# Kernel tuning notes

Hardware: AMD Instinct MI355X
Metric: run time of the kernel (lower is better)

The kernel has to match this reference:

```python
import jax, jax.numpy as jnp
import numpy as np

EPS = 1e-8  # torch.nn.CosineSimilarity default eps


def setup_inputs() -> dict:
    key = jax.random.key(0)
    H, W, C = 2048, 2048, 16
    input_image = jax.random.normal(key, (H, W, 1, C), dtype=jnp.float32)
    return {"input_image": input_image}


def reference(input_image):
    # input_image: [H, W, 1, C] -> per-pixel feature vector of length C
    img = input_image[:, :, 0, :]               # [H, W, C]
    H, W, _ = img.shape
    norms = jnp.sqrt(jnp.sum(img * img, axis=-1))  # [H, W]

    sim = jnp.zeros((H, W), dtype=img.dtype)
    # Original sums cosine sim with the 4 diagonal neighbors (k, l in {-1, 1}),
    # masking out-of-bounds neighbors to 0.
    for dy in (-1, 1):
        for dx in (-1, 1):
            # center pixels m with 0 <= m+dy < H, n with 0 <= n+dx < W
            y0, y1 = max(0, -dy), H - max(0, dy)
            x0, x1 = max(0, -dx), W - max(0, dx)
            a = img[y0:y1, x0:x1]                           # centers
            b = img[y0 + dy:y1 + dy, x0 + dx:x1 + dx]        # diagonal neighbors
            dot = jnp.sum(a * b, axis=-1)
            den = jnp.maximum(norms[y0:y1, x0:x1] *
                              norms[y0 + dy:y1 + dy, x0 + dx:x1 + dx], EPS)
            sim = sim.at[y0:y1, x0:x1].add(dot / den)
    return sim
```

## Files before the change

### kernel.cpp

```cpp
#include <hip/hip_runtime.h>


#define IMG_H 2048
#define IMG_W 2048
#define IMG_C 16

__device__ __forceinline__ float dot4(float4 a, float4 b) {
    return a.x * b.x + a.y * b.y + a.z * b.z + a.w * b.w;
}

__global__ __launch_bounds__(256) void cos_sim_kernel(
    const float* __restrict__ in, float* __restrict__ out) {
    const int x = blockIdx.x * 32 + threadIdx.x;
    const int y = blockIdx.y * 8  + threadIdx.y;

    const float4* v = (const float4*)(in + ((size_t)y * IMG_W + x) * IMG_C);
    const float4 a0 = v[0], a1 = v[1], a2 = v[2], a3 = v[3];
    const float na = dot4(a0, a0) + dot4(a1, a1) + dot4(a2, a2) + dot4(a3, a3);

    float sim = 0.0f;

    #pragma unroll
    for (int k = 0; k < 4; ++k) {
        const int dy = (k & 2) ? 1 : -1;
        const int dx = (k & 1) ? 1 : -1;
        const int ny = y + dy;
        const int nx = x + dx;
        const bool valid = ((unsigned)ny < IMG_H) && ((unsigned)nx < IMG_W);
        const int cy = valid ? ny : y;
        const int cx = valid ? nx : x;
        const float4* u = (const float4*)(in + ((size_t)cy * IMG_W + cx) * IMG_C);
        const float4 b0 = u[0], b1 = u[1], b2 = u[2], b3 = u[3];
        const float dot = dot4(a0, b0) + dot4(a1, b1) + dot4(a2, b2) + dot4(a3, b3);
        const float nb  = dot4(b0, b0) + dot4(b1, b1) + dot4(b2, b2) + dot4(b3, b3);
        const float contrib = dot * rsqrtf(fmaxf(na * nb, 1e-16f));
        sim += valid ? contrib : 0.0f;
    }

    out[(size_t)y * IMG_W + x] = sim;
}

extern "C" void kernel_launch(void* const* d_in, const int* in_sizes, int n_in,
                              void* d_out, int out_size, void* d_ws, size_t ws_size,
                              hipStream_t stream) {
    const float* in = (const float*)d_in[0];
    float* out = (float*)d_out;
    dim3 block(32, 8, 1);
    dim3 grid(IMG_W / 32, IMG_H / 8, 1);
    cos_sim_kernel<<<grid, block, 0, stream>>>(in, out);
}
```

Before: 431.4 us.

## Stage halo tile and per-pixel norms in shared memory for diagonal cosine sim

Each block loads a 34x18 halo tile of 16-channel pixels into LDS with coalesced float4 loads. It computes each pixel's squared norm once into shared memory, then each thread handles two output rows, reading its neighbours from LDS. This removes the redundant global reloads and the repeated norm computation of the per-thread approach. In exchange it uses roughly 50KB of LDS per block, which limits occupancy, and adds halo overhead and two barriers.

```diff
diff --git a/kernel.cpp b/kernel.cpp
--- a/kernel.cpp
+++ b/kernel.cpp
@@ -5,39 +5,84 @@
 #define IMG_W 2048
 #define IMG_C 16
 
+#define TX 32
+#define TY 16
+#define HX (TX + 2)
+#define HY (TY + 2)
+#define NPIX (HX * HY)
+#define PSTRIDE 20
+
 __device__ __forceinline__ float dot4(float4 a, float4 b) {
     return a.x * b.x + a.y * b.y + a.z * b.z + a.w * b.w;
 }
 
 __global__ __launch_bounds__(256) void cos_sim_kernel(
     const float* __restrict__ in, float* __restrict__ out) {
-    const int x = blockIdx.x * 32 + threadIdx.x;
-    const int y = blockIdx.y * 8  + threadIdx.y;
+    __shared__ float tile[NPIX * PSTRIDE];
+    __shared__ float norms[NPIX];
 
-    const float4* v = (const float4*)(in + ((size_t)y * IMG_W + x) * IMG_C);
-    const float4 a0 = v[0], a1 = v[1], a2 = v[2], a3 = v[3];
-    const float na = dot4(a0, a0) + dot4(a1, a1) + dot4(a2, a2) + dot4(a3, a3);
+    const int tid = threadIdx.y * 32 + threadIdx.x;
+    const int bx = blockIdx.x * TX;
+    const int by = blockIdx.y * TY;
 
-    float sim = 0.0f;
+    for (int i = tid; i < NPIX * 4; i += 256) {
+        const int p = i >> 2;
+        const int k = i & 3;
+        const int r = p / HX;
+        const int c = p - r * HX;
+        int gy = by + r - 1;
+        int gx = bx + c - 1;
+        gy = min(max(gy, 0), IMG_H - 1);
+        gx = min(max(gx, 0), IMG_W - 1);
+        const float4 v = *(const float4*)(in + ((size_t)gy * IMG_W + gx) * IMG_C + k * 4);
+        *(float4*)(tile + p * PSTRIDE + k * 4) = v;
+    }
+    __syncthreads();
+
+    for (int p = tid; p < NPIX; p += 256) {
+        const float* t = tile + p * PSTRIDE;
+        const float4 a0 = *(const float4*)(t + 0);
+        const float4 a1 = *(const float4*)(t + 4);
+        const float4 a2 = *(const float4*)(t + 8);
+        const float4 a3 = *(const float4*)(t + 12);
+        norms[p] = dot4(a0, a0) + dot4(a1, a1) + dot4(a2, a2) + dot4(a3, a3);
+    }
+    __syncthreads();
 
     #pragma unroll
-    for (int k = 0; k < 4; ++k) {
-        const int dy = (k & 2) ? 1 : -1;
-        const int dx = (k & 1) ? 1 : -1;
-        const int ny = y + dy;
-        const int nx = x + dx;
-        const bool valid = ((unsigned)ny < IMG_H) && ((unsigned)nx < IMG_W);
-        const int cy = valid ? ny : y;
-        const int cx = valid ? nx : x;
-        const float4* u = (const float4*)(in + ((size_t)cy * IMG_W + cx) * IMG_C);
-        const float4 b0 = u[0], b1 = u[1], b2 = u[2], b3 = u[3];
-        const float dot = dot4(a0, b0) + dot4(a1, b1) + dot4(a2, b2) + dot4(a3, b3);
-        const float nb  = dot4(b0, b0) + dot4(b1, b1) + dot4(b2, b2) + dot4(b3, b3);
-        const float contrib = dot * rsqrtf(fmaxf(na * nb, 1e-16f));
-        sim += valid ? contrib : 0.0f;
+    for (int rr = 0; rr < 2; ++rr) {
+        const int r = threadIdx.y + rr * 8;
+        const int c = threadIdx.x;
+        const int gy = by + r;
+        const int gx = bx + c;
+        const int p = (r + 1) * HX + (c + 1);
+
+        const float* t = tile + p * PSTRIDE;
+        const float4 a0 = *(const float4*)(t + 0);
+        const float4 a1 = *(const float4*)(t + 4);
+        const float4 a2 = *(const float4*)(t + 8);
+        const float4 a3 = *(const float4*)(t + 12);
+        const float na = norms[p];
+
+        float sim = 0.0f;
+        #pragma unroll
+        for (int q = 0; q < 4; ++q) {
+            const int dy = (q & 2) ? 1 : -1;
+            const int dx = (q & 1) ? 1 : -1;
+            const int np = p + dy * HX + dx;
+            const float* u = tile + np * PSTRIDE;
+            const float4 b0 = *(const float4*)(u + 0);
+            const float4 b1 = *(const float4*)(u + 4);
+            const float4 b2 = *(const float4*)(u + 8);
+            const float4 b3 = *(const float4*)(u + 12);
+            const float dot = dot4(a0, b0) + dot4(a1, b1) + dot4(a2, b2) + dot4(a3, b3);
+            const float nb = norms[np];
+            const bool valid = ((unsigned)(gy + dy) < IMG_H) && ((unsigned)(gx + dx) < IMG_W);
+            const float contrib = dot * rsqrtf(fmaxf(na * nb, 1e-16f));
+            sim += valid ? contrib : 0.0f;
+        }
+        out[(size_t)gy * IMG_W + gx] = sim;
     }
-
-    out[(size_t)y * IMG_W + x] = sim;
 }
 
 extern "C" void kernel_launch(void* const* d_in, const int* in_sizes, int n_in,
@@ -46,6 +91,6 @@
     const float* in = (const float*)d_in[0];
     float* out = (float*)d_out;
     dim3 block(32, 8, 1);
-    dim3 grid(IMG_W / 32, IMG_H / 8, 1);
+    dim3 grid(IMG_W / TX, IMG_H / TY, 1);
     cos_sim_kernel<<<grid, block, 0, stream>>>(in, out);
 }
```

New measurement: 370.3 us. -14.2%, faster.
